# Kernel tuning notes

Measured on AMD Instinct MI355X. Metric: run time of the kernel, lower is better.

## Reference

```python
import jax, jax.numpy as jnp
import numpy as np

WS = 14      # window_size
NH = 12      # num_heads


def setup_inputs() -> dict:
    key = jax.random.key(0)
    k0, k1, k2 = jax.random.split(key, 3)
    B, H, W, C = 8, 56, 56, 768
    x = jax.random.normal(k0, (B, H * W, C), jnp.float32)
    s = 1.0 / np.sqrt(C).astype(np.float32)
    w_qkv = jax.random.normal(k1, (C, 3 * C), jnp.float32) * s   # qkv_bias=False
    w_proj = jax.random.normal(k2, (C, C), jnp.float32) * s
    b_proj = jnp.zeros((C,), jnp.float32)
    return {"x": x, "w_qkv": w_qkv, "w_proj": w_proj, "b_proj": b_proj, "H": H, "W": W}


def reference(x, w_qkv, w_proj, b_proj, H, W):
    ws, nh = WS, NH
    B, N, C = x.shape
    hd = C // nh
    H_ = -(-H // ws) * ws
    W_ = -(-W // ws) * ws
    Hn, Wn = H_ // ws, W_ // ws
    L, N_ = Hn * Wn, ws * ws

    qkv = x @ w_qkv                                   # [B, N, 3C]
    qkv = qkv.reshape(B, H, W, 3 * C)
    # pad AFTER the linear, as in the torch code (padded positions have qkv == 0)
    qkv = jnp.pad(qkv, ((0, 0), (0, H_ - H), (0, W_ - W), (0, 0)))
    # window partition: [B,Hn,ws,Wn,ws,3,nh,hd] -> [3,B,L,nh,N_,hd]
    qkv = qkv.reshape(B, Hn, ws, Wn, ws, 3, nh, hd)
    qkv = qkv.transpose(5, 0, 1, 3, 6, 2, 4, 7).reshape(3, B, L, nh, N_, hd)
    q, k, v = qkv[0], qkv[1], qkv[2]

    scale = hd ** -0.5
    attn = jnp.einsum('blhnd,blhmd->blhnm', q * scale, k)   # [B,L,nh,N_,N_]
    attn = jax.nn.softmax(attn, axis=-1)
    out = jnp.einsum('blhnm,blhmd->blhnd', attn, v)          # [B,L,nh,N_,hd]

    # fold windows back: -> [B,H_,W_,C], crop, flatten
    out = out.reshape(B, Hn, Wn, nh, ws, ws, hd)
    out = out.transpose(0, 1, 4, 2, 5, 3, 6).reshape(B, H_, W_, C)
    out = out[:, :H, :W].reshape(B, N, C)
    return out @ w_proj + b_proj
```

## Files before the change

### kernel.cpp

```cpp
#include <hip/hip_runtime.h>

typedef unsigned short u16;
typedef __attribute__((ext_vector_type(8))) __bf16 bf16x8;
typedef __attribute__((ext_vector_type(4))) float floatx4;

__device__ inline float bf2f(u16 u) {
  union { unsigned u; float f; } v; v.u = ((unsigned)u) << 16; return v.f;
}
__device__ inline u16 f2bf(float f) {
  union { float f; unsigned u; } v; v.f = f;
  unsigned r = v.u + 0x7fffu + ((v.u >> 16) & 1u);
  return (u16)(r >> 16);
}

__device__ inline void glds16(const u16* g, u16* l) {
  __builtin_amdgcn_global_load_lds((const __attribute__((address_space(1))) void*)g,
                                   (__attribute__((address_space(3))) void*)l, 16, 0, 0);
}

__global__ __launch_bounds__(256) void detect_k(const u16* __restrict__ w, int* flag)
{
  __shared__ int cnt;
  if (threadIdx.x == 0) cnt = 0;
  __syncthreads();
  int c = 0;
  for (int i = threadIdx.x; i < 16384; i += 256) {
    const int e = (w[i] >> 7) & 0xFF;
    if (e < 64 || e > 191) ++c;
  }
  atomicAdd(&cnt, c);
  __syncthreads();
  if (threadIdx.x == 0) *flag = (cnt > 256) ? 1 : 0;
}

__global__ __launch_bounds__(256) void cast_x_k(const void* __restrict__ in,
                                                u16* __restrict__ out,
                                                int n4, const int* __restrict__ flag)
{
  const int i = blockIdx.x * 256 + threadIdx.x;
  if (i >= n4) return;
  if (*flag) {
    const float4 v = ((const float4*)in)[i];
    u16 o0 = f2bf(v.x), o1 = f2bf(v.y), o2 = f2bf(v.z), o3 = f2bf(v.w);
    uint2 p; p.x = (unsigned)o0 | ((unsigned)o1 << 16); p.y = (unsigned)o2 | ((unsigned)o3 << 16);
    ((uint2*)out)[i] = p;
  } else {
    ((uint2*)out)[i] = ((const uint2*)in)[i];
  }
}

__global__ __launch_bounds__(256) void ct_transpose_k(const void* __restrict__ in,
                                                      u16* __restrict__ out,
                                                      int R, int C, const int* __restrict__ flag)
{
  __shared__ u16 tile[32][33];
  const int f = *flag;
  const int c0 = blockIdx.x * 32, r0 = blockIdx.y * 32;
  const int tx = threadIdx.x & 31, ty = threadIdx.x >> 5;
#pragma unroll
  for (int i = ty; i < 32; i += 8) {
    const size_t idx = (size_t)(r0 + i) * C + (c0 + tx);
    tile[i][tx] = f ? f2bf(((const float*)in)[idx]) : ((const u16*)in)[idx];
  }
  __syncthreads();
#pragma unroll
  for (int i = ty; i < 32; i += 8)
    out[(size_t)(c0 + i) * R + (r0 + tx)] = tile[tx][i];
}

__global__ __launch_bounds__(256) void bias_cast_k(const void* __restrict__ in,
                                                   float* __restrict__ out,
                                                   int n, const int* __restrict__ flag)
{
  const int i = blockIdx.x * 256 + threadIdx.x;
  if (i >= n) return;
  out[i] = *flag ? ((const float*)in)[i] : bf2f(((const u16*)in)[i]);
}

__global__ __launch_bounds__(512, 2) void gemm256(
    const u16* __restrict__ A, const u16* __restrict__ Bt,
    const float* __restrict__ bias, void* __restrict__ C,
    int M, int N, int K, const int* __restrict__ flag, int flagOut)
{
  __shared__ u16 smem[61440];
  u16* As = smem;
  u16* Bs = smem + 28672;
  const int t = threadIdx.x;
  const int wave = t >> 6, lane = t & 63;
  const int quad = lane >> 4, l15 = lane & 15;
  const int wm = wave >> 2, wn = wave & 3;

  const int nwg = gridDim.x;
  const int q = nwg >> 3, r8 = nwg & 7;
  const int xcd = blockIdx.x & 7, loc = blockIdx.x >> 3;
  const int wg = (xcd < r8 ? xcd * (q + 1) : r8 * (q + 1) + (xcd - r8) * q) + loc;
  const int MT = M / 224;
  const int mt = wg % MT, ntile = wg / MT;
  const size_t m0 = (size_t)mt * 224;
  const size_t n0 = (size_t)ntile << 8;

  int addrA[7], addrB[4];
#pragma unroll
  for (int i = 0; i < 7; ++i) {
    const int row = wm * 112 + i * 16 + l15;
    const int hs = (((row & 1) << 2) | quad) ^ ((row >> 1) & 7);
    addrA[i] = (row >> 1) * 64 + hs * 8;
  }
#pragma unroll
  for (int j = 0; j < 4; ++j) {
    const int row = wn * 64 + j * 16 + l15;
    const int hs = (((row & 1) << 2) | quad) ^ ((row >> 1) & 7);
    addrB[j] = (row >> 1) * 64 + hs * 8;
  }

  const u16 *aSrc0, *aSrc1, *bSrc0, *bSrc1;
  {
    const int S0 = t, S1 = 512 + t;
    int line = S0 >> 3, h = (S0 & 7) ^ (line & 7);
    int row = line * 2 + (h >> 2), g = (h & 3) * 8;
    aSrc0 = A + (m0 + row) * (size_t)K + g;
    bSrc0 = Bt + (n0 + row) * (size_t)K + g;
    line = S1 >> 3; h = (S1 & 7) ^ (line & 7);
    row = line * 2 + (h >> 2); g = (h & 3) * 8;
    aSrc1 = A + (m0 + row) * (size_t)K + g;
    bSrc1 = Bt + (n0 + row) * (size_t)K + g;
  }
  const int dst0 = wave * 512;
  const int dst1 = 4096 + wave * 512;

  const int NTk = K >> 5;
  floatx4 acc[7][4] = {};

#pragma unroll
  for (int pt = 0; pt < 2; ++pt) {
    glds16(aSrc0 + pt * 32, As + pt * 7168 + dst0);
    if (wave < 6) glds16(aSrc1 + pt * 32, As + pt * 7168 + dst1);
    glds16(bSrc0 + pt * 32, Bs + pt * 8192 + dst0);
    glds16(bSrc1 + pt * 32, Bs + pt * 8192 + dst1);
  }
  if (wave < 6) asm volatile("s_waitcnt vmcnt(4)" ::: "memory");
  else          asm volatile("s_waitcnt vmcnt(3)" ::: "memory");
  asm volatile("s_barrier" ::: "memory");

  bf16x8 bP[4], a02P[3], bQ[4], a02Q[3];
#pragma unroll
  for (int j = 0; j < 4; ++j) bP[j] = *(const bf16x8*)(Bs + addrB[j]);
#pragma unroll
  for (int i = 0; i < 3; ++i) a02P[i] = *(const bf16x8*)(As + addrA[i]);

#define TILE_BODY(kt, bC, a02C, bN, a02N)                                          \
  {                                                                                \
    const u16* sA_ = As + ((kt) & 3) * 7168;                                       \
    if ((kt) + 2 < NTk) {                                                          \
      const int pre_ = ((kt) + 2) * 32;                                            \
      const int pr_ = ((kt) + 2) & 3;                                              \
      glds16(aSrc0 + pre_, As + pr_ * 7168 + dst0);                                \
      if (wave < 6) glds16(aSrc1 + pre_, As + pr_ * 7168 + dst1);                  \
      glds16(bSrc0 + pre_, Bs + pr_ * 8192 + dst0);                                \
      glds16(bSrc1 + pre_, Bs + pr_ * 8192 + dst1);                                \
    }                                                                              \
    bf16x8 a36_0 = *(const bf16x8*)(sA_ + addrA[3]);                               \
    bf16x8 a36_1 = *(const bf16x8*)(sA_ + addrA[4]);                               \
    bf16x8 a36_2 = *(const bf16x8*)(sA_ + addrA[5]);                               \
    bf16x8 a36_3 = *(const bf16x8*)(sA_ + addrA[6]);                               \
    __builtin_amdgcn_s_setprio(1);                                                 \
    _Pragma("unroll")                                                              \
    for (int i = 0; i < 3; ++i)                                                    \
      _Pragma("unroll")                                                            \
      for (int j = 0; j < 4; ++j)                                                  \
        acc[i][j] = __builtin_amdgcn_mfma_f32_16x16x32_bf16(a02C[i], bC[j], acc[i][j], 0, 0, 0); \
    __builtin_amdgcn_s_setprio(0);                                                 \
    if ((kt) + 2 < NTk) {                                                          \
      if (wave < 6) asm volatile("s_waitcnt vmcnt(4)" ::: "memory");               \
      else          asm volatile("s_waitcnt vmcnt(3)" ::: "memory");               \
      asm volatile("s_barrier" ::: "memory");                                      \
    } else if ((kt) + 1 < NTk) {                                                   \
      asm volatile("s_waitcnt vmcnt(0)" ::: "memory");                             \
      asm volatile("s_barrier" ::: "memory");                                      \
    }                                                                              \
    if ((kt) + 1 < NTk) {                                                          \
      const u16* sAn_ = As + (((kt) + 1) & 3) * 7168;                              \
      const u16* sBn_ = Bs + (((kt) + 1) & 3) * 8192;                              \
      _Pragma("unroll")                                                            \
      for (int j = 0; j < 4; ++j) bN[j] = *(const bf16x8*)(sBn_ + addrB[j]);       \
      _Pragma("unroll")                                                            \
      for (int i = 0; i < 3; ++i) a02N[i] = *(const bf16x8*)(sAn_ + addrA[i]);     \
    }                                                                              \
    __builtin_amdgcn_s_setprio(1);                                                 \
    _Pragma("unroll")                                                              \
    for (int j = 0; j < 4; ++j) {                                                  \
      acc[3][j] = __builtin_amdgcn_mfma_f32_16x16x32_bf16(a36_0, bC[j], acc[3][j], 0, 0, 0); \
      acc[4][j] = __builtin_amdgcn_mfma_f32_16x16x32_bf16(a36_1, bC[j], acc[4][j], 0, 0, 0); \
      acc[5][j] = __builtin_amdgcn_mfma_f32_16x16x32_bf16(a36_2, bC[j], acc[5][j], 0, 0, 0); \
      acc[6][j] = __builtin_amdgcn_mfma_f32_16x16x32_bf16(a36_3, bC[j], acc[6][j], 0, 0, 0); \
    }                                                                              \
    __builtin_amdgcn_s_setprio(0);                                                 \
  }

  for (int kt = 0; kt < NTk; kt += 2) {
    TILE_BODY(kt, bP, a02P, bQ, a02Q);
    TILE_BODY(kt + 1, bQ, a02Q, bP, a02P);
  }
#undef TILE_BODY

  __syncthreads();

  float bvj[4];
#pragma unroll
  for (int j = 0; j < 4; ++j)
    bvj[j] = bias ? bias[n0 + wn * 64 + j * 16 + l15] : 0.0f;

  if (flagOut && (*flag)) {
    float* scrf = (float*)smem + wave * 1088;
    float* Cf = (float*)C;
#pragma unroll
    for (int i = 0; i < 7; ++i) {
#pragma unroll
      for (int j = 0; j < 4; ++j)
#pragma unroll
        for (int rr = 0; rr < 4; ++rr)
          scrf[(quad * 4 + rr) * 68 + j * 16 + l15] = acc[i][j][rr] + bvj[j];
#pragma unroll
      for (int u = lane; u < 256; u += 64) {
        const int row = u >> 4, gr = u & 15;
        float4 vv = *(const float4*)(scrf + row * 68 + gr * 4);
        *(float4*)(Cf + (m0 + wm * 112 + i * 16 + row) * (size_t)N + n0 + wn * 64 + gr * 4) = vv;
      }
    }
  } else {
    u16* scr = smem + wave * 1152;
    u16* Cb = (u16*)C;
#pragma unroll
    for (int i = 0; i < 7; ++i) {
#pragma unroll
      for (int j = 0; j < 4; ++j)
#pragma unroll
        for (int rr = 0; rr < 4; ++rr)
          scr[(quad * 4 + rr) * 72 + j * 16 + l15] = f2bf(acc[i][j][rr] + bvj[j]);
#pragma unroll
      for (int u = lane; u < 128; u += 64) {
        const int row = u >> 3, gr = u & 7;
        int4 vv = *(const int4*)(scr + row * 72 + gr * 8);
        *(int4*)(Cb + (m0 + wm * 112 + i * 16 + row) * (size_t)N + n0 + wn * 64 + gr * 8) = vv;
      }
    }
  }
}

__global__ __launch_bounds__(256, 2) void attn_win(
    const u16* __restrict__ qkv, u16* __restrict__ o)
{
  __shared__ u16 Ks[196 * 64];
  __shared__ u16 Vt[64 * 208];
  __shared__ u16 Pb[4][16 * 208];
  __shared__ int gtok[208];

  const int bid = blockIdx.x;
  const int h = bid % 12;
  const int l = (bid / 12) % 16;
  const int b = bid / 192;
  const int wr0 = (l >> 2) * 14, wc0 = (l & 3) * 14;
  const int baseTok = b * 3136;

  const int t = threadIdx.x, wave = t >> 6, lane = t & 63;
  const int quad = lane >> 4, l15 = lane & 15;

  if (t < 208) {
    const int nn = t < 196 ? t : 195;
    gtok[t] = baseTok + (wr0 + nn / 14) * 56 + wc0 + nn % 14;
  }
  __syncthreads();

  for (int u = t; u < 196 * 8; u += 256) {
    const int row = u >> 3, gg = u & 7;
    int4 kv = *(const int4*)(qkv + (size_t)gtok[row] * 2304 + 768 + h * 64 + gg * 8);
    *(int4*)(Ks + (row * 8 + (gg ^ (row & 7))) * 8) = kv;
  }
  for (int u = t; u < 208 * 8; u += 256) {
    const int n = u >> 3, dg = u & 7;
    int4 vv = {0, 0, 0, 0};
    if (n < 196)
      vv = *(const int4*)(qkv + (size_t)gtok[n] * 2304 + 1536 + h * 64 + dg * 8);
    const u16* pv = (const u16*)&vv;
#pragma unroll
    for (int j = 0; j < 8; ++j) Vt[(dg * 8 + j) * 208 + n] = pv[j];
  }
  __syncthreads();

  u16* Pw = &Pb[wave][0];
  const bf16x8 zerov = {};

  for (int rt = wave; rt < 13; rt += 4) {
    const int n0r = rt * 16;
    int qn = n0r + l15; if (qn > 195) qn = 195;
    const u16* qrow = qkv + (size_t)gtok[qn] * 2304 + h * 64;
    const bf16x8 aq0 = *(const bf16x8*)(qrow + quad * 8);
    const bf16x8 aq1 = *(const bf16x8*)(qrow + 32 + quad * 8);

    floatx4 s[13];
#pragma unroll
    for (int ct = 0; ct < 13; ++ct) {
      int kr = ct * 16 + l15; if (kr > 195) kr = 195;
      const bf16x8 bk0 = *(const bf16x8*)(Ks + (kr * 8 + (quad ^ (kr & 7))) * 8);
      const bf16x8 bk1 = *(const bf16x8*)(Ks + (kr * 8 + ((quad + 4) ^ (kr & 7))) * 8);
      floatx4 z = {};
      z = __builtin_amdgcn_mfma_f32_16x16x32_bf16(aq0, bk0, z, 0, 0, 0);
      z = __builtin_amdgcn_mfma_f32_16x16x32_bf16(aq1, bk1, z, 0, 0, 0);
      s[ct] = z;
    }

    float mx[4], sm[4];
#pragma unroll
    for (int r = 0; r < 4; ++r) mx[r] = -3e38f;
#pragma unroll
    for (int ct = 0; ct < 13; ++ct) {
      const bool maskct = (ct == 12) && (l15 >= 4);
#pragma unroll
      for (int r = 0; r < 4; ++r) {
        float v = s[ct][r] * 0.125f;
        if (maskct) v = -3e38f;
        s[ct][r] = v;
        mx[r] = fmaxf(mx[r], v);
      }
    }
#pragma unroll
    for (int r = 0; r < 4; ++r)
      for (int off = 1; off < 16; off <<= 1)
        mx[r] = fmaxf(mx[r], __shfl_xor(mx[r], off, 64));
#pragma unroll
    for (int r = 0; r < 4; ++r) sm[r] = 0.0f;
#pragma unroll
    for (int ct = 0; ct < 13; ++ct)
#pragma unroll
      for (int r = 0; r < 4; ++r) {
        const float p = __expf(s[ct][r] - mx[r]);
        s[ct][r] = p;
        sm[r] += p;
      }
#pragma unroll
    for (int r = 0; r < 4; ++r)
      for (int off = 1; off < 16; off <<= 1)
        sm[r] += __shfl_xor(sm[r], off, 64);

#pragma unroll
    for (int ct = 0; ct < 13; ++ct)
#pragma unroll
      for (int r = 0; r < 4; ++r)
        Pw[(quad * 4 + r) * 208 + ct * 16 + l15] = f2bf(s[ct][r]);

    floatx4 oacc[4] = {};
#pragma unroll
    for (int ks = 0; ks < 6; ++ks) {
      const bf16x8 ap = *(const bf16x8*)(Pw + l15 * 208 + ks * 32 + quad * 8);
#pragma unroll
      for (int nt = 0; nt < 4; ++nt) {
        const bf16x8 bv = *(const bf16x8*)(Vt + (nt * 16 + l15) * 208 + ks * 32 + quad * 8);
        oacc[nt] = __builtin_amdgcn_mfma_f32_16x16x32_bf16(ap, bv, oacc[nt], 0, 0, 0);
      }
    }
    {
      const int off = 192 + (quad & 1) * 8;
      bf16x8 ap = *(const bf16x8*)(Pw + l15 * 208 + off);
      if (quad >= 2) ap = zerov;
#pragma unroll
      for (int nt = 0; nt < 4; ++nt) {
        const bf16x8 bv = *(const bf16x8*)(Vt + (nt * 16 + l15) * 208 + off);
        oacc[nt] = __builtin_amdgcn_mfma_f32_16x16x32_bf16(ap, bv, oacc[nt], 0, 0, 0);
      }
    }

    float rs[4];
#pragma unroll
    for (int r = 0; r < 4; ++r) rs[r] = 1.0f / sm[r];

#pragma unroll
    for (int nt = 0; nt < 4; ++nt)
#pragma unroll
      for (int r = 0; r < 4; ++r)
        Pw[(quad * 4 + r) * 208 + nt * 16 + l15] = f2bf(oacc[nt][r] * rs[r]);
#pragma unroll
    for (int u = lane; u < 128; u += 64) {
      const int row = u >> 3, gr = u & 7;
      const int n = n0r + row;
      if (n < 196) {
        int4 vv = *(const int4*)(Pw + row * 208 + gr * 8);
        *(int4*)(o + (size_t)gtok[n] * 768 + h * 64 + gr * 8) = vv;
      }
    }
  }
}

extern "C" void kernel_launch(void* const* d_in, const int* in_sizes, int n_in,
                              void* d_out, int out_size, void* d_ws, size_t ws_size,
                              hipStream_t stream)
{
  const void* x     = d_in[0];
  const void* wqkv  = d_in[1];
  const void* wproj = d_in[2];
  const void* bproj = d_in[3];

  char* ws = (char*)d_ws;
  int*   flag   = (int*)ws;
  float* bprojF = (float*)(ws + 16);
  u16*   wqkvT  = (u16*)(ws + 4096);
  u16*   wprojT = (u16*)(ws + 3543040);
  u16*   qkvbuf = (u16*)(ws + 4722688);
  u16*   xb     = (u16*)(ws + 120328192);
  u16*   attno  = xb;

  detect_k<<<1, 256, 0, stream>>>((const u16*)wqkv, flag);
  cast_x_k<<<dim3(18816), 256, 0, stream>>>(x, xb, 4816896, flag);
  ct_transpose_k<<<dim3(72, 24), 256, 0, stream>>>(wqkv, wqkvT, 768, 2304, flag);
  ct_transpose_k<<<dim3(24, 24), 256, 0, stream>>>(wproj, wprojT, 768, 768, flag);
  bias_cast_k<<<dim3(3), 256, 0, stream>>>(bproj, bprojF, 768, flag);

  gemm256<<<dim3(1008), 512, 0, stream>>>(xb, wqkvT, (const float*)nullptr, qkvbuf,
                                          25088, 2304, 768, flag, 0);
  attn_win<<<dim3(1536), 256, 0, stream>>>(qkvbuf, attno);
  gemm256<<<dim3(336), 512, 0, stream>>>(attno, wprojT, bprojF, d_out,
                                         25088, 768, 768, flag, 1);
}
```

Measured before the change: 386.7 us.

## Process GEMM K-tiles in pairs with one barrier per pair

Restructures the GEMM main loop so each iteration consumes two 32-wide K tiles from the 4-slot LDS ring. It prefetches four tiles in the prologue and issues loads for the next pair once per iteration. This halves the number of s_barrier points and interleaves LDS fragment reads between MFMA groups, aiming to cut synchronisation overhead. In exchange, each iteration waits with vmcnt(0) for the whole previous pair, and the loads for a pair go out only one iteration before it is used, which may expose more global-load latency.

```diff
diff --git a/kernel.cpp b/kernel.cpp
--- a/kernel.cpp
+++ b/kernel.cpp
@@ -129,79 +129,88 @@
   const int dst1 = 4096 + wave * 512;
 
   const int NTk = K >> 5;
+  const int NW = NTk >> 1;
   floatx4 acc[7][4] = {};
 
 #pragma unroll
-  for (int pt = 0; pt < 2; ++pt) {
+  for (int pt = 0; pt < 4; ++pt) {
     glds16(aSrc0 + pt * 32, As + pt * 7168 + dst0);
     if (wave < 6) glds16(aSrc1 + pt * 32, As + pt * 7168 + dst1);
     glds16(bSrc0 + pt * 32, Bs + pt * 8192 + dst0);
     glds16(bSrc1 + pt * 32, Bs + pt * 8192 + dst1);
   }
-  if (wave < 6) asm volatile("s_waitcnt vmcnt(4)" ::: "memory");
-  else          asm volatile("s_waitcnt vmcnt(3)" ::: "memory");
+  if (wave < 6) asm volatile("s_waitcnt vmcnt(8)" ::: "memory");
+  else          asm volatile("s_waitcnt vmcnt(6)" ::: "memory");
   asm volatile("s_barrier" ::: "memory");
 
-  bf16x8 bP[4], a02P[3], bQ[4], a02Q[3];
-#pragma unroll
-  for (int j = 0; j < 4; ++j) bP[j] = *(const bf16x8*)(Bs + addrB[j]);
-#pragma unroll
-  for (int i = 0; i < 3; ++i) a02P[i] = *(const bf16x8*)(As + addrA[i]);
-
-#define TILE_BODY(kt, bC, a02C, bN, a02N)                                          \
-  {                                                                                \
-    const u16* sA_ = As + ((kt) & 3) * 7168;                                       \
-    if ((kt) + 2 < NTk) {                                                          \
-      const int pre_ = ((kt) + 2) * 32;                                            \
-      const int pr_ = ((kt) + 2) & 3;                                              \
-      glds16(aSrc0 + pre_, As + pr_ * 7168 + dst0);                                \
-      if (wave < 6) glds16(aSrc1 + pre_, As + pr_ * 7168 + dst1);                  \
-      glds16(bSrc0 + pre_, Bs + pr_ * 8192 + dst0);                                \
-      glds16(bSrc1 + pre_, Bs + pr_ * 8192 + dst1);                                \
-    }                                                                              \
-    bf16x8 a36_0 = *(const bf16x8*)(sA_ + addrA[3]);                               \
-    bf16x8 a36_1 = *(const bf16x8*)(sA_ + addrA[4]);                               \
-    bf16x8 a36_2 = *(const bf16x8*)(sA_ + addrA[5]);                               \
-    bf16x8 a36_3 = *(const bf16x8*)(sA_ + addrA[6]);                               \
-    __builtin_amdgcn_s_setprio(1);                                                 \
-    _Pragma("unroll")                                                              \
-    for (int i = 0; i < 3; ++i)                                                    \
-      _Pragma("unroll")                                                            \
-      for (int j = 0; j < 4; ++j)                                                  \
-        acc[i][j] = __builtin_amdgcn_mfma_f32_16x16x32_bf16(a02C[i], bC[j], acc[i][j], 0, 0, 0); \
-    __builtin_amdgcn_s_setprio(0);                                                 \
-    if ((kt) + 2 < NTk) {                                                          \
-      if (wave < 6) asm volatile("s_waitcnt vmcnt(4)" ::: "memory");               \
-      else          asm volatile("s_waitcnt vmcnt(3)" ::: "memory");               \
-      asm volatile("s_barrier" ::: "memory");                                      \
-    } else if ((kt) + 1 < NTk) {                                                   \
-      asm volatile("s_waitcnt vmcnt(0)" ::: "memory");                             \
-      asm volatile("s_barrier" ::: "memory");                                      \
-    }                                                                              \
-    if ((kt) + 1 < NTk) {                                                          \
-      const u16* sAn_ = As + (((kt) + 1) & 3) * 7168;                              \
-      const u16* sBn_ = Bs + (((kt) + 1) & 3) * 8192;                              \
-      _Pragma("unroll")                                                            \
-      for (int j = 0; j < 4; ++j) bN[j] = *(const bf16x8*)(sBn_ + addrB[j]);       \
-      _Pragma("unroll")                                                            \
-      for (int i = 0; i < 3; ++i) a02N[i] = *(const bf16x8*)(sAn_ + addrA[i]);     \
-    }                                                                              \
-    __builtin_amdgcn_s_setprio(1);                                                 \
-    _Pragma("unroll")                                                              \
-    for (int j = 0; j < 4; ++j) {                                                  \
-      acc[3][j] = __builtin_amdgcn_mfma_f32_16x16x32_bf16(a36_0, bC[j], acc[3][j], 0, 0, 0); \
-      acc[4][j] = __builtin_amdgcn_mfma_f32_16x16x32_bf16(a36_1, bC[j], acc[4][j], 0, 0, 0); \
-      acc[5][j] = __builtin_amdgcn_mfma_f32_16x16x32_bf16(a36_2, bC[j], acc[5][j], 0, 0, 0); \
-      acc[6][j] = __builtin_amdgcn_mfma_f32_16x16x32_bf16(a36_3, bC[j], acc[6][j], 0, 0, 0); \
-    }                                                                              \
-    __builtin_amdgcn_s_setprio(0);                                                 \
-  }
-
-  for (int kt = 0; kt < NTk; kt += 2) {
-    TILE_BODY(kt, bP, a02P, bQ, a02Q);
-    TILE_BODY(kt + 1, bQ, a02Q, bP, a02P);
-  }
-#undef TILE_BODY
+  for (int w = 0; w < NW; ++w) {
+    if (w) asm volatile("s_waitcnt vmcnt(0)\n\ts_barrier" ::: "memory");
+
+    const int e = 2 * w;
+    const u16* sAe = As + (e & 3) * 7168;
+    const u16* sBe = Bs + (e & 3) * 8192;
+    const u16* sAo = As + ((e + 1) & 3) * 7168;
+    const u16* sBo = Bs + ((e + 1) & 3) * 8192;
+
+    if (w && e + 2 < NTk) {
+      const int e2 = e + 2, o2 = e + 3;
+      glds16(aSrc0 + e2 * 32, As + (e2 & 3) * 7168 + dst0);
+      if (wave < 6) glds16(aSrc1 + e2 * 32, As + (e2 & 3) * 7168 + dst1);
+      glds16(bSrc0 + e2 * 32, Bs + (e2 & 3) * 8192 + dst0);
+      glds16(bSrc1 + e2 * 32, Bs + (e2 & 3) * 8192 + dst1);
+      glds16(aSrc0 + o2 * 32, As + (o2 & 3) * 7168 + dst0);
+      if (wave < 6) glds16(aSrc1 + o2 * 32, As + (o2 & 3) * 7168 + dst1);
+      glds16(bSrc0 + o2 * 32, Bs + (o2 & 3) * 8192 + dst0);
+      glds16(bSrc1 + o2 * 32, Bs + (o2 & 3) * 8192 + dst1);
+    }
+
+    bf16x8 bP[4], a02P[3], a36P[4];
+#pragma unroll
+    for (int j = 0; j < 4; ++j) bP[j] = *(const bf16x8*)(sBe + addrB[j]);
+#pragma unroll
+    for (int i = 0; i < 3; ++i) a02P[i] = *(const bf16x8*)(sAe + addrA[i]);
+#pragma unroll
+    for (int i = 0; i < 4; ++i) a36P[i] = *(const bf16x8*)(sAe + addrA[3 + i]);
+
+    __builtin_amdgcn_s_setprio(1);
+#pragma unroll
+    for (int i = 0; i < 3; ++i)
+#pragma unroll
+      for (int j = 0; j < 4; ++j)
+        acc[i][j] = __builtin_amdgcn_mfma_f32_16x16x32_bf16(a02P[i], bP[j], acc[i][j], 0, 0, 0);
+    __builtin_amdgcn_s_setprio(0);
+
+    bf16x8 bQ[4], a02Q[3];
+#pragma unroll
+    for (int j = 0; j < 4; ++j) bQ[j] = *(const bf16x8*)(sBo + addrB[j]);
+#pragma unroll
+    for (int i = 0; i < 3; ++i) a02Q[i] = *(const bf16x8*)(sAo + addrA[i]);
+
+    __builtin_amdgcn_s_setprio(1);
+#pragma unroll
+    for (int i = 0; i < 4; ++i)
+#pragma unroll
+      for (int j = 0; j < 4; ++j)
+        acc[3 + i][j] = __builtin_amdgcn_mfma_f32_16x16x32_bf16(a36P[i], bP[j], acc[3 + i][j], 0, 0, 0);
+    __builtin_amdgcn_s_setprio(0);
+
+    bf16x8 a36Q[4];
+#pragma unroll
+    for (int i = 0; i < 4; ++i) a36Q[i] = *(const bf16x8*)(sAo + addrA[3 + i]);
+
+    __builtin_amdgcn_s_setprio(1);
+#pragma unroll
+    for (int i = 0; i < 3; ++i)
+#pragma unroll
+      for (int j = 0; j < 4; ++j)
+        acc[i][j] = __builtin_amdgcn_mfma_f32_16x16x32_bf16(a02Q[i], bQ[j], acc[i][j], 0, 0, 0);
+#pragma unroll
+    for (int i = 0; i < 4; ++i)
+#pragma unroll
+      for (int j = 0; j < 4; ++j)
+        acc[3 + i][j] = __builtin_amdgcn_mfma_f32_16x16x32_bf16(a36Q[i], bQ[j], acc[3 + i][j], 0, 0, 0);
+    __builtin_amdgcn_s_setprio(0);
+  }
 
   __syncthreads();
 
```

Result: no change. 390.8 us (+1.1%).
